# Kernel tuning notes

Hardware: AMD Instinct MI355X
Metric: run time of the kernel (lower is better)

Reference implementation:

```python
import jax, jax.numpy as jnp
import numpy as np

N_SIDE = 7
N_NODES = N_SIDE * N_SIDE  # 49


def _grid_edge_index(h, w):
    # torch_geometric.utils.grid: 9-point stencil (8 neighbors + self-loop)
    src, dst = [], []
    for y in range(h):
        for x in range(w):
            for dy in (-1, 0, 1):
                for dx in (-1, 0, 1):
                    ny, nx = y + dy, x + dx
                    if 0 <= ny < h and 0 <= nx < w:
                        src.append(ny * w + nx)
                        dst.append(y * w + x)
    return np.stack([np.array(src), np.array(dst)]).astype(np.int64)


def _gcn_norm_adj(edge_index, n):
    # PyG GCNConv default: add self-loops (on top of any existing), weight 1,
    # deg = in-degree by edge weight, A_hat = D^-1/2 (A + I) D^-1/2
    src, dst = edge_index[0], edge_index[1]
    A = jnp.zeros((n, n), dtype=jnp.float32).at[dst, src].add(1.0)
    A = A + jnp.eye(n, dtype=jnp.float32)  # GCNConv's added self-loops
    deg = A.sum(axis=1)
    d_inv_sqrt = jnp.where(deg > 0, jax.lax.rsqrt(deg), 0.0)
    return A * d_inv_sqrt[:, None] * d_inv_sqrt[None, :]  # [n, n]


def setup_inputs() -> dict:
    key = jax.random.key(0)
    ks = jax.random.split(key, 4)
    B = 4096
    features = jax.random.normal(ks[0], (B, N_NODES, 768), dtype=jnp.float32)
    W1 = jax.random.normal(ks[1], (768, 256), dtype=jnp.float32) * (1.0 / np.sqrt(768))
    b1 = jnp.zeros((256,), dtype=jnp.float32)
    W2 = jax.random.normal(ks[2], (256, 128), dtype=jnp.float32) * (1.0 / np.sqrt(256))
    b2 = jnp.zeros((128,), dtype=jnp.float32)
    fcW = jax.random.normal(ks[3], (128, 4), dtype=jnp.float32) * (1.0 / np.sqrt(128))
    fcb = jnp.zeros((4,), dtype=jnp.float32)
    edge_index = jnp.asarray(_grid_edge_index(N_SIDE, N_SIDE))  # [2, 361]
    return {"features": features, "W1": W1, "b1": b1, "W2": W2, "b2": b2,
            "fcW": fcW, "fcb": fcb, "edge_index": edge_index}


def reference(features, W1, b1, W2, b2, fcW, fcb, edge_index):
    # features: [B, N, 768]; batched GCN over the shared 7x7 grid graph
    A_hat = _gcn_norm_adj(edge_index, N_NODES)  # [N, N]
    # GCNConv: aggregate(X @ W) + b
    h = jnp.einsum('mn,bnd->bmd', A_hat, features @ W1) + b1  # [B, N, 256]
    h = jax.nn.relu(h)
    h = jnp.einsum('mn,bnd->bmd', A_hat, h @ W2) + b2  # [B, N, 128]
    h = jax.nn.relu(h)
    pooled = h.mean(axis=1)  # [B, 128] mean over nodes
    return pooled @ fcW + fcb  # [B, 4]
```

## Files before the change

kernel.cpp:

```cpp
#include <hip/hip_runtime.h>

#define NN 49
#define D0 768
#define D1 256
#define D2 128

typedef short v8s __attribute__((ext_vector_type(8)));
typedef float v4f __attribute__((ext_vector_type(4)));
typedef int   v4i __attribute__((ext_vector_type(4)));

__device__ __forceinline__ unsigned short f2bf(float f) {
  unsigned int u = __float_as_uint(f);
  u += 0x7FFFu + ((u >> 16) & 1u);
  return (unsigned short)(u >> 16);
}
__device__ __forceinline__ float bf2f(unsigned short u) {
  return __uint_as_float((unsigned)u << 16);
}

__device__ __forceinline__ int permk(int k) {
  return (k & ~31) | ((k & 12) << 1) | ((k & 16) >> 2) | (k & 3);
}

__device__ __forceinline__ float ahat(int m, int k) {
  if (m >= NN || k >= NN) return 0.f;
  int ym = m / 7, xm = m % 7, yk = k / 7, xk = k % 7;
  int dy = ym - yk, dx = xm - xk;
  if (dy < -1 || dy > 1 || dx < -1 || dx > 1) return 0.f;
  float rm = rsqrtf((float)((1 + (ym > 0) + (ym < 6)) * (1 + (xm > 0) + (xm < 6))) + 1.0f);
  float rk = rsqrtf((float)((1 + (yk > 0) + (yk < 6)) * (1 + (xk > 0) + (xk < 6))) + 1.0f);
  return ((m == k) ? 2.0f : 1.0f) * rm * rk;
}

#define W1_IMG_BYTES 393216
#define WS_NEEDED    458752

__global__ void prep_w(const float* __restrict__ W1, const float* __restrict__ W2,
                       char* __restrict__ wimg) {
  int id = blockIdx.x * 256 + threadIdx.x;
  if (id < 24576) {
    int kc = id >> 11, p = (id >> 8) & 7, tt = id & 255;
    int wvv = tt >> 6, lnn = tt & 63, qq = lnn >> 4, lmm = lnn & 15;
    int nt = p >> 1, s = p & 1;
    int n  = 64 * wvv + 16 * nt + lmm;
    int k0 = kc * 64 + 32 * s + 4 * qq;
    v8s v;
    #pragma unroll
    for (int i = 0; i < 4; ++i) {
      v[i]     = (short)f2bf(W1[(size_t)(k0 + i) * D1 + n]);
      v[i + 4] = (short)f2bf(W1[(size_t)(k0 + 16 + i) * D1 + n]);
    }
    *(v8s*)(wimg + (size_t)id * 16) = v;
  }
  int id2 = id - 24576;
  if (id2 >= 0 && id2 < 4096) {
    int kc = id2 >> 10, p = (id2 >> 8) & 3, tt = id2 & 255;
    int wvv = tt >> 6, lnn = tt & 63, qq = lnn >> 4, lmm = lnn & 15;
    int nt = p >> 1, s = p & 1;
    int n  = 32 * wvv + 16 * nt + lmm;
    int k0 = kc * 64 + 32 * s + 4 * qq;
    v8s v;
    #pragma unroll
    for (int i = 0; i < 4; ++i) {
      v[i]     = (short)f2bf(W2[(size_t)(k0 + i) * D2 + n]);
      v[i + 4] = (short)f2bf(W2[(size_t)(k0 + 16 + i) * D2 + n]);
    }
    *(v8s*)(wimg + W1_IMG_BYTES + (size_t)id2 * 16) = v;
  }
}

#define NOFF_SX    0
#define NOFF_SPOOL 0
#define NOFF_SH1   16384
#define NSMEM_SZ   49152

__device__ __forceinline__ void ldw8(v8s* dst, const char* base) {
  #pragma unroll
  for (int p = 0; p < 8; ++p) dst[p] = *(const v8s*)(base + p * 4096);
}
__device__ __forceinline__ void ldw4(v8s* dst, const char* base) {
  #pragma unroll
  for (int p = 0; p < 4; ++p) dst[p] = *(const v8s*)(base + p * 4096);
}

__device__ __forceinline__ void mfma_phase1(v4f (&acc)[4][4], const char* sx,
                                            const v8s* w, int q, int lm) {
  #pragma unroll
  for (int ks = 0; ks < 2; ++ks) {
    const int off = ks * 64 + (q << 4);
    v8s af[4];
    #pragma unroll
    for (int mt = 0; mt < 4; ++mt) {
      int row = mt * 16 + lm;
      af[mt] = *(const v8s*)(sx + ((row * 128 + off) ^ ((row & 7) << 4)));
    }
    #pragma unroll
    for (int mt = 0; mt < 4; ++mt)
      #pragma unroll
      for (int nt = 0; nt < 4; ++nt)
        acc[mt][nt] = __builtin_amdgcn_mfma_f32_16x16x32_bf16(af[mt], w[2 * nt + ks], acc[mt][nt], 0, 0, 0);
  }
}

__global__ __launch_bounds__(256, 2) void gcn_fused6(
    const float* __restrict__ X, const char* __restrict__ wimg,
    const float* __restrict__ b1v, const float* __restrict__ b2v,
    const float* __restrict__ fcWv, const float* __restrict__ fcbv,
    float* __restrict__ out)
{
  __shared__ __align__(16) char smem[NSMEM_SZ];
  const int t  = threadIdx.x;
  const int wv = t >> 6;
  const int ln = t & 63;
  const int q  = ln >> 4;
  const int lm = ln & 15;

  if (t < 240) {
    int i = (t >= 120) ? t - 120 : t;
    int base = ((t >= 120) ? 8192 : 0) + 6272 + i * 16;
    *(v4i*)(smem + NOFF_SX + base) = (v4i){0, 0, 0, 0};
  }

  const float* Xb = X + (size_t)blockIdx.x * (NN * D0);

  const int segA = t;
  const int segB = t + 256;
  const bool actB = (segB < NN * 8);
  const int rowA = segA >> 3, fA = segA & 7;
  const int rowB = segB >> 3, fB = segB & 7;
  const int gofsA = rowA * D0 + 32 * (fA >> 2) + 4 * (fA & 3);
  const int gofsB_ = rowB * D0 + 32 * (fB >> 2) + 4 * (fB & 3);
  const int gofsB = actB ? gofsB_ : gofsA;
  const int ldsA = (rowA * 128 + 16 * fA) ^ ((rowA & 7) << 4);
  const int ldsB = (rowB * 128 + 16 * fB) ^ ((rowB & 7) << 4);

  const int tofs = t * 16;
  const char* w1img = wimg;

  v4f acc[4][4];
  #pragma unroll
  for (int i = 0; i < 4; ++i)
    #pragma unroll
    for (int j = 0; j < 4; ++j)
      acc[i][j] = (v4f){0.f, 0.f, 0.f, 0.f};

  v8s wA[8], wB[8];
  ldw8(wA, w1img + tofs);
  float4 xa0 = *(const float4*)(Xb + gofsA);
  float4 xa1 = *(const float4*)(Xb + gofsA + 16);
  float4 xb0 = *(const float4*)(Xb + gofsB);
  float4 xb1 = *(const float4*)(Xb + gofsB + 16);

  for (int kc2 = 0; kc2 < 12; kc2 += 2) {
    {
      v8s v;
      v[0] = (short)f2bf(xa0.x); v[1] = (short)f2bf(xa0.y);
      v[2] = (short)f2bf(xa0.z); v[3] = (short)f2bf(xa0.w);
      v[4] = (short)f2bf(xa1.x); v[5] = (short)f2bf(xa1.y);
      v[6] = (short)f2bf(xa1.z); v[7] = (short)f2bf(xa1.w);
      *(v8s*)(smem + NOFF_SX + ldsA) = v;
      if (actB) {
        v8s w;
        w[0] = (short)f2bf(xb0.x); w[1] = (short)f2bf(xb0.y);
        w[2] = (short)f2bf(xb0.z); w[3] = (short)f2bf(xb0.w);
        w[4] = (short)f2bf(xb1.x); w[5] = (short)f2bf(xb1.y);
        w[6] = (short)f2bf(xb1.z); w[7] = (short)f2bf(xb1.w);
        *(v8s*)(smem + NOFF_SX + ldsB) = w;
      }
    }
    {
      const float* xp = Xb + (kc2 + 1) * 64;
      xa0 = *(const float4*)(xp + gofsA);
      xa1 = *(const float4*)(xp + gofsA + 16);
      xb0 = *(const float4*)(xp + gofsB);
      xb1 = *(const float4*)(xp + gofsB + 16);
      ldw8(wB, w1img + (kc2 + 1) * 32768 + tofs);
    }
    __builtin_amdgcn_sched_barrier(0);
    asm volatile("s_waitcnt lgkmcnt(0)" ::: "memory");
    __builtin_amdgcn_s_barrier();
    __builtin_amdgcn_sched_barrier(0);
    mfma_phase1(acc, smem + NOFF_SX, wA, q, lm);

    {
      v8s v;
      v[0] = (short)f2bf(xa0.x); v[1] = (short)f2bf(xa0.y);
      v[2] = (short)f2bf(xa0.z); v[3] = (short)f2bf(xa0.w);
      v[4] = (short)f2bf(xa1.x); v[5] = (short)f2bf(xa1.y);
      v[6] = (short)f2bf(xa1.z); v[7] = (short)f2bf(xa1.w);
      *(v8s*)(smem + NOFF_SX + 8192 + ldsA) = v;
      if (actB) {
        v8s w;
        w[0] = (short)f2bf(xb0.x); w[1] = (short)f2bf(xb0.y);
        w[2] = (short)f2bf(xb0.z); w[3] = (short)f2bf(xb0.w);
        w[4] = (short)f2bf(xb1.x); w[5] = (short)f2bf(xb1.y);
        w[6] = (short)f2bf(xb1.z); w[7] = (short)f2bf(xb1.w);
        *(v8s*)(smem + NOFF_SX + 8192 + ldsB) = w;
      }
    }
    if (kc2 < 10) {
      const float* xp = Xb + (kc2 + 2) * 64;
      xa0 = *(const float4*)(xp + gofsA);
      xa1 = *(const float4*)(xp + gofsA + 16);
      xb0 = *(const float4*)(xp + gofsB);
      xb1 = *(const float4*)(xp + gofsB + 16);
      ldw8(wA, w1img + (kc2 + 2) * 32768 + tofs);
    }
    __builtin_amdgcn_sched_barrier(0);
    asm volatile("s_waitcnt lgkmcnt(0)" ::: "memory");
    __builtin_amdgcn_s_barrier();
    __builtin_amdgcn_sched_barrier(0);
    mfma_phase1(acc, smem + NOFF_SX + 8192, wB, q, lm);
  }

  const char* w2img = wimg + W1_IMG_BYTES;
  v8s w2c[4][4];
  ldw4(w2c[0], w2img + tofs);
  ldw4(w2c[1], w2img + 16384 + tofs);

  float bi[4];
  #pragma unroll
  for (int nt = 0; nt < 4; ++nt) bi[nt] = b1v[64 * wv + 16 * nt + lm];

  v8s afH[4][2], afL[4][2];
  #pragma unroll
  for (int mt = 0; mt < 4; ++mt) {
    int m = 16 * mt + lm;
    #pragma unroll
    for (int s2 = 0; s2 < 2; ++s2) {
      v8s hi, lo;
      #pragma unroll
      for (int j = 0; j < 8; ++j) {
        int k = 32 * s2 + ((j & 4) << 2) + 4 * q + (j & 3);
        float v = ahat(m, k);
        unsigned short h = f2bf(v);
        hi[j] = (short)h;
        lo[j] = (short)f2bf(v - bf2f(h));
      }
      afH[mt][s2] = hi; afL[mt][s2] = lo;
    }
  }

  v4f ag[4][4];
  #pragma unroll
  for (int mt = 0; mt < 4; ++mt)
    #pragma unroll
    for (int nt = 0; nt < 4; ++nt)
      ag[mt][nt] = (v4f){bi[nt], bi[nt], bi[nt], bi[nt]};

  #pragma unroll
  for (int s2 = 0; s2 < 2; ++s2)
    #pragma unroll
    for (int nt = 0; nt < 4; ++nt) {
      v8s b;
      #pragma unroll
      for (int i = 0; i < 4; ++i) {
        b[i]     = (short)f2bf(acc[2 * s2][nt][i]);
        b[i + 4] = (short)f2bf(acc[2 * s2 + 1][nt][i]);
      }
      #pragma unroll
      for (int mt = 0; mt < 4; ++mt) {
        ag[mt][nt] = __builtin_amdgcn_mfma_f32_16x16x32_bf16(afL[mt][s2], b, ag[mt][nt], 0, 0, 0);
        ag[mt][nt] = __builtin_amdgcn_mfma_f32_16x16x32_bf16(afH[mt][s2], b, ag[mt][nt], 0, 0, 0);
      }
    }

  ldw4(w2c[2], w2img + 2 * 16384 + tofs);
  ldw4(w2c[3], w2img + 3 * 16384 + tofs);

  #pragma unroll
  for (int mt = 0; mt < 4; ++mt)
    #pragma unroll
    for (int nt = 0; nt < 4; ++nt) {
      int ch  = 64 * wv + 16 * nt + lm;
      int chb = 2 * permk(ch);
      #pragma unroll
      for (int r = 0; r < 4; ++r) {
        int row = 16 * mt + 4 * q + r;
        float hv = fmaxf(ag[mt][nt][r], 0.f);
        int byte = (row * 512 + chb) ^ ((row & 7) << 4);
        *(unsigned short*)(smem + NOFF_SH1 + byte) = f2bf(hv);
      }
    }
  __builtin_amdgcn_sched_barrier(0);
  asm volatile("s_waitcnt lgkmcnt(0)" ::: "memory");
  __builtin_amdgcn_s_barrier();
  __builtin_amdgcn_sched_barrier(0);

  v4f acc3[4][2];
  #pragma unroll
  for (int i = 0; i < 4; ++i) { acc3[i][0] = (v4f){0.f,0.f,0.f,0.f}; acc3[i][1] = (v4f){0.f,0.f,0.f,0.f}; }

  #pragma unroll
  for (int kc = 0; kc < 4; ++kc)
    #pragma unroll
    for (int ks = 0; ks < 2; ++ks) {
      const int off = ks * 64 + (q << 4);
      v8s af[4];
      #pragma unroll
      for (int mt = 0; mt < 4; ++mt) {
        int row = mt * 16 + lm;
        int byte = (row * 512 + kc * 128 + off) ^ ((row & 7) << 4);
        af[mt] = *(const v8s*)(smem + NOFF_SH1 + byte);
      }
      #pragma unroll
      for (int mt = 0; mt < 4; ++mt)
        #pragma unroll
        for (int nt = 0; nt < 2; ++nt)
          acc3[mt][nt] = __builtin_amdgcn_mfma_f32_16x16x32_bf16(af[mt], w2c[kc][2 * nt + ks], acc3[mt][nt], 0, 0, 0);
    }

  float b2i[2];
  b2i[0] = b2v[32 * wv + lm];
  b2i[1] = b2v[32 * wv + 16 + lm];
  v4f a2[4][2];
  #pragma unroll
  for (int mt = 0; mt < 4; ++mt) {
    a2[mt][0] = (v4f){b2i[0], b2i[0], b2i[0], b2i[0]};
    a2[mt][1] = (v4f){b2i[1], b2i[1], b2i[1], b2i[1]};
  }
  #pragma unroll
  for (int s2 = 0; s2 < 2; ++s2)
    #pragma unroll
    for (int nt = 0; nt < 2; ++nt) {
      v8s b;
      #pragma unroll
      for (int i = 0; i < 4; ++i) {
        b[i]     = (short)f2bf(acc3[2 * s2][nt][i]);
        b[i + 4] = (short)f2bf(acc3[2 * s2 + 1][nt][i]);
      }
      #pragma unroll
      for (int mt = 0; mt < 4; ++mt) {
        a2[mt][nt] = __builtin_amdgcn_mfma_f32_16x16x32_bf16(afL[mt][s2], b, a2[mt][nt], 0, 0, 0);
        a2[mt][nt] = __builtin_amdgcn_mfma_f32_16x16x32_bf16(afH[mt][s2], b, a2[mt][nt], 0, 0, 0);
      }
    }

  float ps0 = 0.f, ps1 = 0.f;
  #pragma unroll
  for (int mt = 0; mt < 3; ++mt)
    #pragma unroll
    for (int r = 0; r < 4; ++r) {
      ps0 += fmaxf(a2[mt][0][r], 0.f);
      ps1 += fmaxf(a2[mt][1][r], 0.f);
    }
  if (q == 0) {
    ps0 += fmaxf(a2[3][0][0], 0.f);
    ps1 += fmaxf(a2[3][1][0], 0.f);
  }
  ps0 += __shfl_xor(ps0, 16); ps0 += __shfl_xor(ps0, 32);
  ps1 += __shfl_xor(ps1, 16); ps1 += __shfl_xor(ps1, 32);
  float* spool = (float*)(smem + NOFF_SPOOL);
  __syncthreads();
  if (q == 0) {
    spool[32 * wv + lm]      = ps0 * (1.0f / 49.0f);
    spool[32 * wv + 16 + lm] = ps1 * (1.0f / 49.0f);
  }
  __syncthreads();
  if (t < 4) {
    float a = fcbv[t];
    for (int d = 0; d < D2; ++d) a += spool[d] * fcWv[d * 4 + t];
    out[(size_t)blockIdx.x * 4 + t] = a;
  }
}

#define OFF_SX    0
#define OFF_SWT   8192
#define OFF_SC    0
#define OFF_SWT2  0
#define OFF_SPOOL 25872
#define OFF_SPF   30096
#define OFF_SH1   40960
#define OFF_NBRW  73728
#define OFF_NBRI  75492
#define OFF_B1    77256
#define OFF_B2    78280
#define OFF_FCW   78792
#define OFF_FCB   80840
#define SMEM_SZ   80856

__global__ __launch_bounds__(256, 2) void gcn_fused_fb(
    const float* __restrict__ X, const float* __restrict__ W1,
    const float* __restrict__ b1v, const float* __restrict__ W2,
    const float* __restrict__ b2v, const float* __restrict__ fcWv,
    const float* __restrict__ fcbv, float* __restrict__ out)
{
  __shared__ __align__(16) char smem[SMEM_SZ];
  const int t  = threadIdx.x;
  const int wv = t >> 6;
  const int ln = t & 63;
  const int q  = ln >> 4;
  const int lm = ln & 15;

  float* nbrW = (float*)(smem + OFF_NBRW);
  int*   nbrI = (int*)  (smem + OFF_NBRI);
  float* b1s  = (float*)(smem + OFF_B1);
  float* b2s  = (float*)(smem + OFF_B2);
  float* fcWs = (float*)(smem + OFF_FCW);
  float* fcbs = (float*)(smem + OFF_FCB);
  float* sC   = (float*)(smem + OFF_SC);

  if (t < D1) b1s[t] = b1v[t];
  if (t < D2) b2s[t] = b2v[t];
  fcWs[t]       = fcWv[t];
  fcWs[t + 256] = fcWv[t + 256];
  if (t < 4) fcbs[t] = fcbv[t];
  if (t < NN) {
    int y = t / 7, x = t % 7;
    float rm = rsqrtf((float)((1 + (y > 0) + (y < 6)) * (1 + (x > 0) + (x < 6))) + 1.0f);
    int cnt = 0;
    for (int dy = -1; dy <= 1; ++dy)
      for (int dx = -1; dx <= 1; ++dx) {
        int ny = y + dy, nx = x + dx;
        if (ny >= 0 && ny < 7 && nx >= 0 && nx < 7) {
          int n = ny * 7 + nx;
          float rn = rsqrtf((float)((1 + (ny > 0) + (ny < 6)) * (1 + (nx > 0) + (nx < 6))) + 1.0f);
          nbrW[t * 9 + cnt] = ((n == t) ? 2.0f : 1.0f) * rm * rn;
          nbrI[t * 9 + cnt] = n;
          ++cnt;
        }
      }
    for (; cnt < 9; ++cnt) { nbrW[t * 9 + cnt] = 0.0f; nbrI[t * 9 + cnt] = 0; }
  }
  __syncthreads();

  const float* Xb = X + (size_t)blockIdx.x * (NN * D0);
  v4f acc[4][4];
  #pragma unroll
  for (int i = 0; i < 4; ++i)
    #pragma unroll
    for (int j = 0; j < 4; ++j)
      acc[i][j] = (v4f){0.f, 0.f, 0.f, 0.f};

  for (int kc = 0; kc < 12; ++kc) {
    __syncthreads();
    #pragma unroll
    for (int p = 0; p < 4; ++p) {
      int idx = t + 256 * p;
      int row = idx >> 4;
      int k4  = (idx & 15) << 2;
      float4 v = {0.f, 0.f, 0.f, 0.f};
      if (row < NN) v = *(const float4*)(Xb + row * D0 + kc * 64 + k4);
      ushort4 s;
      s.x = f2bf(v.x); s.y = f2bf(v.y); s.z = f2bf(v.z); s.w = f2bf(v.w);
      int byte = row * 128 + 2 * permk(k4);
      byte ^= (row & 7) << 4;
      *(ushort4*)(smem + OFF_SX + byte) = s;
    }
    #pragma unroll
    for (int p = 0; p < 4; ++p) {
      int bid2 = t + 256 * p;
      int k0 = (bid2 & 15) << 2;
      int n0 = (bid2 >> 4) << 2;
      const float* wp = W1 + (size_t)(kc * 64 + k0) * D1 + n0;
      float4 r0 = *(const float4*)(wp);
      float4 r1 = *(const float4*)(wp + D1);
      float4 r2 = *(const float4*)(wp + 2 * D1);
      float4 r3 = *(const float4*)(wp + 3 * D1);
      int kb = 2 * permk(k0);
      ushort4 s; int byte;
      s.x = f2bf(r0.x); s.y = f2bf(r1.x); s.z = f2bf(r2.x); s.w = f2bf(r3.x);
      byte = (n0 + 0) * 128 + kb; byte ^= ((n0 + 0) & 7) << 4;
      *(ushort4*)(smem + OFF_SWT + byte) = s;
      s.x = f2bf(r0.y); s.y = f2bf(r1.y); s.z = f2bf(r2.y); s.w = f2bf(r3.y);
      byte = (n0 + 1) * 128 + kb; byte ^= ((n0 + 1) & 7) << 4;
      *(ushort4*)(smem + OFF_SWT + byte) = s;
      s.x = f2bf(r0.z); s.y = f2bf(r1.z); s.z = f2bf(r2.z); s.w = f2bf(r3.z);
      byte = (n0 + 2) * 128 + kb; byte ^= ((n0 + 2) & 7) << 4;
      *(ushort4*)(smem + OFF_SWT + byte) = s;
      s.x = f2bf(r0.w); s.y = f2bf(r1.w); s.z = f2bf(r2.w); s.w = f2bf(r3.w);
      byte = (n0 + 3) * 128 + kb; byte ^= ((n0 + 3) & 7) << 4;
      *(ushort4*)(smem + OFF_SWT + byte) = s;
    }
    __syncthreads();
    #pragma unroll
    for (int ks = 0; ks < 2; ++ks) {
      int off = ks * 64 + (q << 4);
      v8s af[4], bf[4];
      #pragma unroll
      for (int mt = 0; mt < 4; ++mt) {
        int row = mt * 16 + lm;
        int byte = row * 128 + off; byte ^= (row & 7) << 4;
        af[mt] = *(const v8s*)(smem + OFF_SX + byte);
      }
      #pragma unroll
      for (int nt = 0; nt < 4; ++nt) {
        int n = (wv * 4 + nt) * 16 + lm;
        int byte = n * 128 + off; byte ^= (n & 7) << 4;
        bf[nt] = *(const v8s*)(smem + OFF_SWT + byte);
      }
      #pragma unroll
      for (int mt = 0; mt < 4; ++mt)
        #pragma unroll
        for (int nt = 0; nt < 4; ++nt)
          acc[mt][nt] = __builtin_amdgcn_mfma_f32_16x16x32_bf16(af[mt], bf[nt], acc[mt][nt], 0, 0, 0);
    }
  }

  #pragma unroll
  for (int h = 0; h < 2; ++h) {
    __syncthreads();
    if ((wv >> 1) == h) {
      #pragma unroll
      for (int mt = 0; mt < 4; ++mt) {
        int rbase = mt * 16 + (q << 2);
        #pragma unroll
        for (int nt = 0; nt < 4; ++nt) {
          int c = ((wv & 1) * 4 + nt) * 16 + lm;
          #pragma unroll
          for (int r = 0; r < 4; ++r) {
            int row = rbase + r;
            if (row < NN) sC[row * 132 + c] = acc[mt][nt][r];
          }
        }
      }
    }
    __syncthreads();
    for (int p = 0; p < 7; ++p) {
      int idx = t + 256 * p;
      if (idx < NN * 32) {
        int m  = idx >> 5;
        int d4 = (idx & 31) << 2;
        int dg = h * 128 + d4;
        float a0 = b1s[dg], a1 = b1s[dg + 1], a2 = b1s[dg + 2], a3 = b1s[dg + 3];
        #pragma unroll
        for (int e = 0; e < 9; ++e) {
          float w = nbrW[m * 9 + e];
          int   n = nbrI[m * 9 + e];
          float4 cv = *(const float4*)(sC + n * 132 + d4);
          a0 += w * cv.x; a1 += w * cv.y; a2 += w * cv.z; a3 += w * cv.w;
        }
        a0 = fmaxf(a0, 0.f); a1 = fmaxf(a1, 0.f); a2 = fmaxf(a2, 0.f); a3 = fmaxf(a3, 0.f);
        ushort4 s; s.x = f2bf(a0); s.y = f2bf(a1); s.z = f2bf(a2); s.w = f2bf(a3);
        int byte = m * 512 + 2 * permk(dg);
        byte ^= (m & 7) << 4;
        *(ushort4*)(smem + OFF_SH1 + byte) = s;
      }
    }
  }

  v4f acc2[4][2];
  #pragma unroll
  for (int i = 0; i < 4; ++i) { acc2[i][0] = (v4f){0.f,0.f,0.f,0.f}; acc2[i][1] = (v4f){0.f,0.f,0.f,0.f}; }

  for (int kc = 0; kc < 4; ++kc) {
    __syncthreads();
    #pragma unroll
    for (int p = 0; p < 2; ++p) {
      int bid2 = t + 256 * p;
      int k0 = (bid2 & 15) << 2;
      int n0 = (bid2 >> 4) << 2;
      const float* wp = W2 + (size_t)(kc * 64 + k0) * D2 + n0;
      float4 r0 = *(const float4*)(wp);
      float4 r1 = *(const float4*)(wp + D2);
      float4 r2 = *(const float4*)(wp + 2 * D2);
      float4 r3 = *(const float4*)(wp + 3 * D2);
      int kb = 2 * permk(k0);
      ushort4 s; int byte;
      s.x = f2bf(r0.x); s.y = f2bf(r1.x); s.z = f2bf(r2.x); s.w = f2bf(r3.x);
      byte = (n0 + 0) * 128 + kb; byte ^= ((n0 + 0) & 7) << 4;
      *(ushort4*)(smem + OFF_SWT2 + byte) = s;
      s.x = f2bf(r0.y); s.y = f2bf(r1.y); s.z = f2bf(r2.y); s.w = f2bf(r3.y);
      byte = (n0 + 1) * 128 + kb; byte ^= ((n0 + 1) & 7) << 4;
      *(ushort4*)(smem + OFF_SWT2 + byte) = s;
      s.x = f2bf(r0.z); s.y = f2bf(r1.z); s.z = f2bf(r2.z); s.w = f2bf(r3.z);
      byte = (n0 + 2) * 128 + kb; byte ^= ((n0 + 2) & 7) << 4;
      *(ushort4*)(smem + OFF_SWT2 + byte) = s;
      s.x = f2bf(r0.w); s.y = f2bf(r1.w); s.z = f2bf(r2.w); s.w = f2bf(r3.w);
      byte = (n0 + 3) * 128 + kb; byte ^= ((n0 + 3) & 7) << 4;
      *(ushort4*)(smem + OFF_SWT2 + byte) = s;
    }
    __syncthreads();
    #pragma unroll
    for (int ks = 0; ks < 2; ++ks) {
      int off = ks * 64 + (q << 4);
      v8s af[4], bf2[2];
      #pragma unroll
      for (int mt = 0; mt < 4; ++mt) {
        int row = mt * 16 + lm;
        int byte = row * 512 + kc * 128 + off; byte ^= (row & 7) << 4;
        af[mt] = *(const v8s*)(smem + OFF_SH1 + byte);
      }
      #pragma unroll
      for (int nt = 0; nt < 2; ++nt) {
        int n = (wv * 2 + nt) * 16 + lm;
        int byte = n * 128 + off; byte ^= (n & 7) << 4;
        bf2[nt] = *(const v8s*)(smem + OFF_SWT2 + byte);
      }
      #pragma unroll
      for (int mt = 0; mt < 4; ++mt)
        #pragma unroll
        for (int nt = 0; nt < 2; ++nt)
          acc2[mt][nt] = __builtin_amdgcn_mfma_f32_16x16x32_bf16(af[mt], bf2[nt], acc2[mt][nt], 0, 0, 0);
    }
  }

  __syncthreads();
  #pragma unroll
  for (int mt = 0; mt < 4; ++mt) {
    int rbase = mt * 16 + (q << 2);
    #pragma unroll
    for (int nt = 0; nt < 2; ++nt) {
      int c = (wv * 2 + nt) * 16 + lm;
      #pragma unroll
      for (int r = 0; r < 4; ++r) {
        int row = rbase + r;
        if (row < NN) sC[row * 132 + c] = acc2[mt][nt][r];
      }
    }
  }
  __syncthreads();
  {
    int d4 = (t & 31) << 2;
    int g  = t >> 5;
    float p0 = 0.f, p1 = 0.f, p2 = 0.f, p3 = 0.f;
    int m0 = g * 7, m1 = (g * 7 + 7 < NN) ? (g * 7 + 7) : NN;
    for (int m = m0; m < m1; ++m) {
      float a0 = b2s[d4], a1 = b2s[d4 + 1], a2 = b2s[d4 + 2], a3 = b2s[d4 + 3];
      #pragma unroll
      for (int e = 0; e < 9; ++e) {
        float w = nbrW[m * 9 + e];
        int   n = nbrI[m * 9 + e];
        float4 cv = *(const float4*)(sC + n * 132 + d4);
        a0 += w * cv.x; a1 += w * cv.y; a2 += w * cv.z; a3 += w * cv.w;
      }
      p0 += fmaxf(a0, 0.f); p1 += fmaxf(a1, 0.f); p2 += fmaxf(a2, 0.f); p3 += fmaxf(a3, 0.f);
    }
    float* sp = (float*)(smem + OFF_SPOOL) + g * 132 + d4;
    sp[0] = p0; sp[1] = p1; sp[2] = p2; sp[3] = p3;
  }
  __syncthreads();
  if (t < D2) {
    const float* sp = (const float*)(smem + OFF_SPOOL);
    float s = 0.f;
    #pragma unroll
    for (int g = 0; g < 8; ++g) s += sp[g * 132 + t];
    ((float*)(smem + OFF_SPF))[t] = s * (1.0f / 49.0f);
  }
  __syncthreads();
  if (t < 4) {
    const float* pf = (const float*)(smem + OFF_SPF);
    float a = fcbs[t];
    for (int d = 0; d < D2; ++d) a += pf[d] * fcWs[d * 4 + t];
    out[(size_t)blockIdx.x * 4 + t] = a;
  }
}

extern "C" void kernel_launch(void* const* d_in, const int* in_sizes, int n_in,
                              void* d_out, int out_size, void* d_ws, size_t ws_size,
                              hipStream_t stream) {
  const float* X   = (const float*)d_in[0];
  const float* W1  = (const float*)d_in[1];
  const float* b1  = (const float*)d_in[2];
  const float* W2  = (const float*)d_in[3];
  const float* b2  = (const float*)d_in[4];
  const float* fcW = (const float*)d_in[5];
  const float* fcb = (const float*)d_in[6];
  float* out = (float*)d_out;
  int B = in_sizes[0] / (NN * D0);
  if (d_ws != nullptr && ws_size >= (size_t)WS_NEEDED) {
    prep_w<<<112, 256, 0, stream>>>(W1, W2, (char*)d_ws);
    gcn_fused6<<<B, 256, 0, stream>>>(X, (const char*)d_ws, b1, b2, fcW, fcb, out);
  } else {
    gcn_fused_fb<<<B, 256, 0, stream>>>(X, W1, b1, W2, b2, fcW, fcb, out);
  }
}
```

Before: 224.0 us.

## Process two graphs per block to share W1/W2 register fragments

Each block now handles two batch samples instead of one. The W1 fragments loaded into registers per k-chunk, and the W2 fragments, are reused for both samples' MFMAs, which halves weight traffic per sample. The X staging loop becomes single-buffered with one LDS slot per sample, and shared memory grows to 80KB to hold both samples' hidden activations. The trade-off is that LDS double-buffering across k-chunks is lost, the grid is halved, and register pressure and LDS use rise, which could reduce occupancy.

```diff
diff --git a/kernel.cpp b/kernel.cpp
--- a/kernel.cpp
+++ b/kernel.cpp
@@ -39,11 +39,11 @@
                        char* __restrict__ wimg) {
   int id = blockIdx.x * 256 + threadIdx.x;
   if (id < 24576) {
-    int kc = id >> 11, p = (id >> 8) & 7, tt = id & 255;
+    int p = (id >> 8) & 7, tt = id & 255;
     int wvv = tt >> 6, lnn = tt & 63, qq = lnn >> 4, lmm = lnn & 15;
     int nt = p >> 1, s = p & 1;
     int n  = 64 * wvv + 16 * nt + lmm;
-    int k0 = kc * 64 + 32 * s + 4 * qq;
+    int k0 = (id >> 11) * 64 + 32 * s + 4 * qq;
     v8s v;
     #pragma unroll
     for (int i = 0; i < 4; ++i) {
@@ -54,11 +54,11 @@
   }
   int id2 = id - 24576;
   if (id2 >= 0 && id2 < 4096) {
-    int kc = id2 >> 10, p = (id2 >> 8) & 3, tt = id2 & 255;
+    int p = (id2 >> 8) & 3, tt = id2 & 255;
     int wvv = tt >> 6, lnn = tt & 63, qq = lnn >> 4, lmm = lnn & 15;
     int nt = p >> 1, s = p & 1;
     int n  = 32 * wvv + 16 * nt + lmm;
-    int k0 = kc * 64 + 32 * s + 4 * qq;
+    int k0 = (id2 >> 10) * 64 + 32 * s + 4 * qq;
     v8s v;
     #pragma unroll
     for (int i = 0; i < 4; ++i) {
@@ -69,10 +69,13 @@
   }
 }
 
-#define NOFF_SX    0
-#define NOFF_SPOOL 0
-#define NOFF_SH1   16384
-#define NSMEM_SZ   49152
+#define SX0    0
+#define SX1    8192
+#define SH1_0  16384
+#define SH1_1  49152
+#define SPOOL0 0
+#define SPOOL1 512
+#define NSMEM7 81920
 
 __device__ __forceinline__ void ldw8(v8s* dst, const char* base) {
   #pragma unroll
@@ -82,33 +85,22 @@
   #pragma unroll
   for (int p = 0; p < 4; ++p) dst[p] = *(const v8s*)(base + p * 4096);
 }
-
-__device__ __forceinline__ void mfma_phase1(v4f (&acc)[4][4], const char* sx,
-                                            const v8s* w, int q, int lm) {
-  #pragma unroll
-  for (int ks = 0; ks < 2; ++ks) {
-    const int off = ks * 64 + (q << 4);
-    v8s af[4];
-    #pragma unroll
-    for (int mt = 0; mt < 4; ++mt) {
-      int row = mt * 16 + lm;
-      af[mt] = *(const v8s*)(sx + ((row * 128 + off) ^ ((row & 7) << 4)));
-    }
-    #pragma unroll
-    for (int mt = 0; mt < 4; ++mt)
-      #pragma unroll
-      for (int nt = 0; nt < 4; ++nt)
-        acc[mt][nt] = __builtin_amdgcn_mfma_f32_16x16x32_bf16(af[mt], w[2 * nt + ks], acc[mt][nt], 0, 0, 0);
-  }
-}
-
-__global__ __launch_bounds__(256, 2) void gcn_fused6(
+__device__ __forceinline__ void commit8(char* lds, const float4& a, const float4& b) {
+  v8s v;
+  v[0] = (short)f2bf(a.x); v[1] = (short)f2bf(a.y);
+  v[2] = (short)f2bf(a.z); v[3] = (short)f2bf(a.w);
+  v[4] = (short)f2bf(b.x); v[5] = (short)f2bf(b.y);
+  v[6] = (short)f2bf(b.z); v[7] = (short)f2bf(b.w);
+  *(v8s*)lds = v;
+}
+
+__global__ __launch_bounds__(256, 2) void gcn_fused8(
     const float* __restrict__ X, const char* __restrict__ wimg,
     const float* __restrict__ b1v, const float* __restrict__ b2v,
     const float* __restrict__ fcWv, const float* __restrict__ fcbv,
     float* __restrict__ out)
 {
-  __shared__ __align__(16) char smem[NSMEM_SZ];
+  __shared__ __align__(16) char smem[NSMEM7];
   const int t  = threadIdx.x;
   const int wv = t >> 6;
   const int ln = t & 63;
@@ -117,106 +109,124 @@
 
   if (t < 240) {
     int i = (t >= 120) ? t - 120 : t;
-    int base = ((t >= 120) ? 8192 : 0) + 6272 + i * 16;
-    *(v4i*)(smem + NOFF_SX + base) = (v4i){0, 0, 0, 0};
-  }
-
-  const float* Xb = X + (size_t)blockIdx.x * (NN * D0);
-
-  const int segA = t;
-  const int segB = t + 256;
-  const bool actB = (segB < NN * 8);
-  const int rowA = segA >> 3, fA = segA & 7;
-  const int rowB = segB >> 3, fB = segB & 7;
-  const int gofsA = rowA * D0 + 32 * (fA >> 2) + 4 * (fA & 3);
-  const int gofsB_ = rowB * D0 + 32 * (fB >> 2) + 4 * (fB & 3);
-  const int gofsB = actB ? gofsB_ : gofsA;
-  const int ldsA = (rowA * 128 + 16 * fA) ^ ((rowA & 7) << 4);
-  const int ldsB = (rowB * 128 + 16 * fB) ^ ((rowB & 7) << 4);
+    int base = ((t >= 120) ? SX1 : SX0) + 6272 + i * 16;
+    *(v4i*)(smem + base) = (v4i){0, 0, 0, 0};
+  }
+
+  const float* X0 = X + (size_t)(2 * blockIdx.x) * (NN * D0);
+  const float* X1 = X0 + NN * D0;
+
+  const int g1 = t + 256;
+  const int b1g = (g1 >= 392) ? 1 : 0;
+  const bool act3 = (t < 16);
+  const int s0 = t, s1 = g1 - 392 * b1g, s2 = t + 120, s3 = t + 376;
+  const int r0 = s0 >> 3, f0 = s0 & 7;
+  const int r1 = s1 >> 3, f1 = s1 & 7;
+  const int r2 = s2 >> 3, f2 = s2 & 7;
+  const int r3 = s3 >> 3, f3 = s3 & 7;
+  const float* base0 = X0 + r0 * D0 + 32 * (f0 >> 2) + 4 * (f0 & 3);
+  const float* base1 = (b1g ? X1 : X0) + r1 * D0 + 32 * (f1 >> 2) + 4 * (f1 & 3);
+  const float* base2 = X1 + r2 * D0 + 32 * (f2 >> 2) + 4 * (f2 & 3);
+  const float* base3_ = X1 + r3 * D0 + 32 * (f3 >> 2) + 4 * (f3 & 3);
+  const float* base3 = act3 ? base3_ : base0;
+  const int lds0 = SX0 + ((r0 * 128 + 16 * f0) ^ ((r0 & 7) << 4));
+  const int lds1 = (b1g ? SX1 : SX0) + ((r1 * 128 + 16 * f1) ^ ((r1 & 7) << 4));
+  const int lds2 = SX1 + ((r2 * 128 + 16 * f2) ^ ((r2 & 7) << 4));
+  const int lds3 = SX1 + (((r3 & 63) * 128 + 16 * f3) ^ ((r3 & 7) << 4));
 
   const int tofs = t * 16;
-  const char* w1img = wimg;
-
-  v4f acc[4][4];
+
+  v4f accA[4][4], accB[4][4];
   #pragma unroll
   for (int i = 0; i < 4; ++i)
     #pragma unroll
-    for (int j = 0; j < 4; ++j)
-      acc[i][j] = (v4f){0.f, 0.f, 0.f, 0.f};
-
-  v8s wA[8], wB[8];
-  ldw8(wA, w1img + tofs);
-  float4 xa0 = *(const float4*)(Xb + gofsA);
-  float4 xa1 = *(const float4*)(Xb + gofsA + 16);
-  float4 xb0 = *(const float4*)(Xb + gofsB);
-  float4 xb1 = *(const float4*)(Xb + gofsB + 16);
-
-  for (int kc2 = 0; kc2 < 12; kc2 += 2) {
-    {
-      v8s v;
-      v[0] = (short)f2bf(xa0.x); v[1] = (short)f2bf(xa0.y);
-      v[2] = (short)f2bf(xa0.z); v[3] = (short)f2bf(xa0.w);
-      v[4] = (short)f2bf(xa1.x); v[5] = (short)f2bf(xa1.y);
-      v[6] = (short)f2bf(xa1.z); v[7] = (short)f2bf(xa1.w);
-      *(v8s*)(smem + NOFF_SX + ldsA) = v;
-      if (actB) {
-        v8s w;
-        w[0] = (short)f2bf(xb0.x); w[1] = (short)f2bf(xb0.y);
-        w[2] = (short)f2bf(xb0.z); w[3] = (short)f2bf(xb0.w);
-        w[4] = (short)f2bf(xb1.x); w[5] = (short)f2bf(xb1.y);
-        w[6] = (short)f2bf(xb1.z); w[7] = (short)f2bf(xb1.w);
-        *(v8s*)(smem + NOFF_SX + ldsB) = w;
-      }
-    }
-    {
-      const float* xp = Xb + (kc2 + 1) * 64;
-      xa0 = *(const float4*)(xp + gofsA);
-      xa1 = *(const float4*)(xp + gofsA + 16);
-      xb0 = *(const float4*)(xp + gofsB);
-      xb1 = *(const float4*)(xp + gofsB + 16);
-      ldw8(wB, w1img + (kc2 + 1) * 32768 + tofs);
+    for (int j = 0; j < 4; ++j) {
+      accA[i][j] = (v4f){0.f, 0.f, 0.f, 0.f};
+      accB[i][j] = (v4f){0.f, 0.f, 0.f, 0.f};
+    }
+
+  v8s wA[8];
+  ldw8(wA, wimg + tofs);
+  float4 p0a = *(const float4*)(base0);
+  float4 p0b = *(const float4*)(base0 + 16);
+  float4 p1a = *(const float4*)(base1);
+  float4 p1b = *(const float4*)(base1 + 16);
+  float4 p2a = *(const float4*)(base2);
+  float4 p2b = *(const float4*)(base2 + 16);
+  float4 p3a = *(const float4*)(base3);
+  float4 p3b = *(const float4*)(base3 + 16);
+
+  for (int kc = 0; kc < 12; ++kc) {
+    __builtin_amdgcn_sched_barrier(0);
+    __builtin_amdgcn_s_barrier();
+    __builtin_amdgcn_sched_barrier(0);
+    commit8((char*)smem + lds0, p0a, p0b);
+    commit8((char*)smem + lds1, p1a, p1b);
+    commit8((char*)smem + lds2, p2a, p2b);
+    if (act3) commit8((char*)smem + lds3, p3a, p3b);
+    if (kc < 11) {
+      const int o = (kc + 1) * 64;
+      p0a = *(const float4*)(base0 + o);
+      p0b = *(const float4*)(base0 + o + 16);
+      p1a = *(const float4*)(base1 + o);
+      p1b = *(const float4*)(base1 + o + 16);
+      p2a = *(const float4*)(base2 + o);
+      p2b = *(const float4*)(base2 + o + 16);
+      p3a = *(const float4*)(base3 + o);
+      p3b = *(const float4*)(base3 + o + 16);
     }
     __builtin_amdgcn_sched_barrier(0);
     asm volatile("s_waitcnt lgkmcnt(0)" ::: "memory");
     __builtin_amdgcn_s_barrier();
     __builtin_amdgcn_sched_barrier(0);
-    mfma_phase1(acc, smem + NOFF_SX, wA, q, lm);
-
-    {
-      v8s v;
-      v[0] = (short)f2bf(xa0.x); v[1] = (short)f2bf(xa0.y);
-      v[2] = (short)f2bf(xa0.z); v[3] = (short)f2bf(xa0.w);
-      v[4] = (short)f2bf(xa1.x); v[5] = (short)f2bf(xa1.y);
-      v[6] = (short)f2bf(xa1.z); v[7] = (short)f2bf(xa1.w);
-      *(v8s*)(smem + NOFF_SX + 8192 + ldsA) = v;
-      if (actB) {
-        v8s w;
-        w[0] = (short)f2bf(xb0.x); w[1] = (short)f2bf(xb0.y);
-        w[2] = (short)f2bf(xb0.z); w[3] = (short)f2bf(xb0.w);
-        w[4] = (short)f2bf(xb1.x); w[5] = (short)f2bf(xb1.y);
-        w[6] = (short)f2bf(xb1.z); w[7] = (short)f2bf(xb1.w);
-        *(v8s*)(smem + NOFF_SX + 8192 + ldsB) = w;
-      }
-    }
-    if (kc2 < 10) {
-      const float* xp = Xb + (kc2 + 2) * 64;
-      xa0 = *(const float4*)(xp + gofsA);
-      xa1 = *(const float4*)(xp + gofsA + 16);
-      xb0 = *(const float4*)(xp + gofsB);
-      xb1 = *(const float4*)(xp + gofsB + 16);
-      ldw8(wA, w1img + (kc2 + 2) * 32768 + tofs);
-    }
-    __builtin_amdgcn_sched_barrier(0);
-    asm volatile("s_waitcnt lgkmcnt(0)" ::: "memory");
-    __builtin_amdgcn_s_barrier();
-    __builtin_amdgcn_sched_barrier(0);
-    mfma_phase1(acc, smem + NOFF_SX + 8192, wB, q, lm);
-  }
-
-  const char* w2img = wimg + W1_IMG_BYTES;
-  v8s w2c[4][4];
-  ldw4(w2c[0], w2img + tofs);
-  ldw4(w2c[1], w2img + 16384 + tofs);
+    #pragma unroll
+    for (int ks = 0; ks < 2; ++ks) {
+      const int off = ks * 64 + (q << 4);
+      v8s af[4];
+      #pragma unroll
+      for (int mt = 0; mt < 4; ++mt) {
+        int row = mt * 16 + lm;
+        af[mt] = *(const v8s*)(smem + SX0 + ((row * 128 + off) ^ ((row & 7) << 4)));
+      }
+      #pragma unroll
+      for (int mt = 0; mt < 4; ++mt)
+        #pragma unroll
+        for (int nt = 0; nt < 4; ++nt)
+          accA[mt][nt] = __builtin_amdgcn_mfma_f32_16x16x32_bf16(af[mt], wA[2 * nt + ks], accA[mt][nt], 0, 0, 0);
+    }
+    #pragma unroll
+    for (int ks = 0; ks < 2; ++ks) {
+      const int off = ks * 64 + (q << 4);
+      v8s af[4];
+      #pragma unroll
+      for (int mt = 0; mt < 4; ++mt) {
+        int row = mt * 16 + lm;
+        af[mt] = *(const v8s*)(smem + SX1 + ((row * 128 + off) ^ ((row & 7) << 4)));
+      }
+      #pragma unroll
+      for (int mt = 0; mt < 4; ++mt)
+        #pragma unroll
+        for (int nt = 0; nt < 4; ++nt)
+          accB[mt][nt] = __builtin_amdgcn_mfma_f32_16x16x32_bf16(af[mt], wA[2 * nt + ks], accB[mt][nt], 0, 0, 0);
+    }
+    if (kc < 11) ldw8(wA, wimg + (kc + 1) * 32768 + tofs);
+  }
+
+  v8s bA[2][4], bB[2][4];
+  #pragma unroll
+  for (int s2 = 0; s2 < 2; ++s2)
+    #pragma unroll
+    for (int nt = 0; nt < 4; ++nt) {
+      v8s a, b;
+      #pragma unroll
+      for (int i = 0; i < 4; ++i) {
+        a[i]     = (short)f2bf(accA[2 * s2][nt][i]);
+        a[i + 4] = (short)f2bf(accA[2 * s2 + 1][nt][i]);
+        b[i]     = (short)f2bf(accB[2 * s2][nt][i]);
+        b[i + 4] = (short)f2bf(accB[2 * s2 + 1][nt][i]);
+      }
+      bA[s2][nt] = a; bB[s2][nt] = b;
+    }
 
   float bi[4];
   #pragma unroll
@@ -241,126 +251,134 @@
     }
   }
 
-  v4f ag[4][4];
-  #pragma unroll
-  for (int mt = 0; mt < 4; ++mt)
-    #pragma unroll
-    for (int nt = 0; nt < 4; ++nt)
-      ag[mt][nt] = (v4f){bi[nt], bi[nt], bi[nt], bi[nt]};
-
-  #pragma unroll
-  for (int s2 = 0; s2 < 2; ++s2)
-    #pragma unroll
-    for (int nt = 0; nt < 4; ++nt) {
-      v8s b;
-      #pragma unroll
-      for (int i = 0; i < 4; ++i) {
-        b[i]     = (short)f2bf(acc[2 * s2][nt][i]);
-        b[i + 4] = (short)f2bf(acc[2 * s2 + 1][nt][i]);
-      }
-      #pragma unroll
-      for (int mt = 0; mt < 4; ++mt) {
-        ag[mt][nt] = __builtin_amdgcn_mfma_f32_16x16x32_bf16(afL[mt][s2], b, ag[mt][nt], 0, 0, 0);
-        ag[mt][nt] = __builtin_amdgcn_mfma_f32_16x16x32_bf16(afH[mt][s2], b, ag[mt][nt], 0, 0, 0);
-      }
-    }
-
-  ldw4(w2c[2], w2img + 2 * 16384 + tofs);
-  ldw4(w2c[3], w2img + 3 * 16384 + tofs);
-
-  #pragma unroll
-  for (int mt = 0; mt < 4; ++mt)
-    #pragma unroll
-    for (int nt = 0; nt < 4; ++nt) {
-      int ch  = 64 * wv + 16 * nt + lm;
-      int chb = 2 * permk(ch);
-      #pragma unroll
-      for (int r = 0; r < 4; ++r) {
-        int row = 16 * mt + 4 * q + r;
-        float hv = fmaxf(ag[mt][nt][r], 0.f);
-        int byte = (row * 512 + chb) ^ ((row & 7) << 4);
-        *(unsigned short*)(smem + NOFF_SH1 + byte) = f2bf(hv);
-      }
-    }
+  #pragma unroll
+  for (int bb = 0; bb < 2; ++bb) {
+    v4f ag[4][4];
+    #pragma unroll
+    for (int mt = 0; mt < 4; ++mt)
+      #pragma unroll
+      for (int nt = 0; nt < 4; ++nt)
+        ag[mt][nt] = (v4f){bi[nt], bi[nt], bi[nt], bi[nt]};
+    #pragma unroll
+    for (int s2 = 0; s2 < 2; ++s2)
+      #pragma unroll
+      for (int nt = 0; nt < 4; ++nt) {
+        v8s b = (bb == 0) ? bA[s2][nt] : bB[s2][nt];
+        #pragma unroll
+        for (int mt = 0; mt < 4; ++mt) {
+          ag[mt][nt] = __builtin_amdgcn_mfma_f32_16x16x32_bf16(afL[mt][s2], b, ag[mt][nt], 0, 0, 0);
+          ag[mt][nt] = __builtin_amdgcn_mfma_f32_16x16x32_bf16(afH[mt][s2], b, ag[mt][nt], 0, 0, 0);
+        }
+      }
+    const int hbase = (bb == 0) ? SH1_0 : SH1_1;
+    #pragma unroll
+    for (int mt = 0; mt < 4; ++mt)
+      #pragma unroll
+      for (int nt = 0; nt < 4; ++nt) {
+        int ch  = 64 * wv + 16 * nt + lm;
+        int chb = 2 * permk(ch);
+        #pragma unroll
+        for (int r = 0; r < 4; ++r) {
+          int row = 16 * mt + 4 * q + r;
+          float hv = fmaxf(ag[mt][nt][r], 0.f);
+          int byte = (row * 512 + chb) ^ ((row & 7) << 4);
+          *(unsigned short*)(smem + hbase + byte) = f2bf(hv);
+        }
+      }
+  }
+
+  const char* w2img = wimg + W1_IMG_BYTES;
+  v8s w2c0[4], w2c1[4], w2c2[4], w2c3[4];
+  ldw4(w2c0, w2img + tofs);
+  ldw4(w2c1, w2img + 16384 + tofs);
+  ldw4(w2c2, w2img + 2 * 16384 + tofs);
+  ldw4(w2c3, w2img + 3 * 16384 + tofs);
+
   __builtin_amdgcn_sched_barrier(0);
   asm volatile("s_waitcnt lgkmcnt(0)" ::: "memory");
   __builtin_amdgcn_s_barrier();
   __builtin_amdgcn_sched_barrier(0);
 
-  v4f acc3[4][2];
-  #pragma unroll
-  for (int i = 0; i < 4; ++i) { acc3[i][0] = (v4f){0.f,0.f,0.f,0.f}; acc3[i][1] = (v4f){0.f,0.f,0.f,0.f}; }
-
-  #pragma unroll
-  for (int kc = 0; kc < 4; ++kc)
-    #pragma unroll
-    for (int ks = 0; ks < 2; ++ks) {
-      const int off = ks * 64 + (q << 4);
-      v8s af[4];
-      #pragma unroll
-      for (int mt = 0; mt < 4; ++mt) {
-        int row = mt * 16 + lm;
-        int byte = (row * 512 + kc * 128 + off) ^ ((row & 7) << 4);
-        af[mt] = *(const v8s*)(smem + NOFF_SH1 + byte);
-      }
-      #pragma unroll
-      for (int mt = 0; mt < 4; ++mt)
-        #pragma unroll
-        for (int nt = 0; nt < 2; ++nt)
-          acc3[mt][nt] = __builtin_amdgcn_mfma_f32_16x16x32_bf16(af[mt], w2c[kc][2 * nt + ks], acc3[mt][nt], 0, 0, 0);
-    }
-
-  float b2i[2];
-  b2i[0] = b2v[32 * wv + lm];
-  b2i[1] = b2v[32 * wv + 16 + lm];
-  v4f a2[4][2];
-  #pragma unroll
-  for (int mt = 0; mt < 4; ++mt) {
-    a2[mt][0] = (v4f){b2i[0], b2i[0], b2i[0], b2i[0]};
-    a2[mt][1] = (v4f){b2i[1], b2i[1], b2i[1], b2i[1]};
-  }
-  #pragma unroll
-  for (int s2 = 0; s2 < 2; ++s2)
-    #pragma unroll
-    for (int nt = 0; nt < 2; ++nt) {
-      v8s b;
-      #pragma unroll
-      for (int i = 0; i < 4; ++i) {
-        b[i]     = (short)f2bf(acc3[2 * s2][nt][i]);
-        b[i + 4] = (short)f2bf(acc3[2 * s2 + 1][nt][i]);
-      }
-      #pragma unroll
-      for (int mt = 0; mt < 4; ++mt) {
-        a2[mt][nt] = __builtin_amdgcn_mfma_f32_16x16x32_bf16(afL[mt][s2], b, a2[mt][nt], 0, 0, 0);
-        a2[mt][nt] = __builtin_amdgcn_mfma_f32_16x16x32_bf16(afH[mt][s2], b, a2[mt][nt], 0, 0, 0);
-      }
-    }
-
-  float ps0 = 0.f, ps1 = 0.f;
-  #pragma unroll
-  for (int mt = 0; mt < 3; ++mt)
-    #pragma unroll
-    for (int r = 0; r < 4; ++r) {
-      ps0 += fmaxf(a2[mt][0][r], 0.f);
-      ps1 += fmaxf(a2[mt][1][r], 0.f);
-    }
-  if (q == 0) {
-    ps0 += fmaxf(a2[3][0][0], 0.f);
-    ps1 += fmaxf(a2[3][1][0], 0.f);
-  }
-  ps0 += __shfl_xor(ps0, 16); ps0 += __shfl_xor(ps0, 32);
-  ps1 += __shfl_xor(ps1, 16); ps1 += __shfl_xor(ps1, 32);
-  float* spool = (float*)(smem + NOFF_SPOOL);
+  float b2i0 = b2v[32 * wv + lm];
+  float b2i1 = b2v[32 * wv + 16 + lm];
+
+  #pragma unroll
+  for (int bb = 0; bb < 2; ++bb) {
+    const int hbase = (bb == 0) ? SH1_0 : SH1_1;
+    v4f acc3[4][2];
+    #pragma unroll
+    for (int i = 0; i < 4; ++i) {
+      acc3[i][0] = (v4f){0.f, 0.f, 0.f, 0.f};
+      acc3[i][1] = (v4f){0.f, 0.f, 0.f, 0.f};
+    }
+    #pragma unroll
+    for (int kc = 0; kc < 4; ++kc)
+      #pragma unroll
+      for (int ks = 0; ks < 2; ++ks) {
+        const int off = ks * 64 + (q << 4);
+        v8s af[4];
+        #pragma unroll
+        for (int mt = 0; mt < 4; ++mt) {
+          int row = mt * 16 + lm;
+          int byte = (row * 512 + kc * 128 + off) ^ ((row & 7) << 4);
+          af[mt] = *(const v8s*)(smem + hbase + byte);
+        }
+        const v8s* wc = (kc == 0) ? w2c0 : (kc == 1) ? w2c1 : (kc == 2) ? w2c2 : w2c3;
+        #pragma unroll
+        for (int mt = 0; mt < 4; ++mt)
+          #pragma unroll
+          for (int nt = 0; nt < 2; ++nt)
+            acc3[mt][nt] = __builtin_amdgcn_mfma_f32_16x16x32_bf16(af[mt], wc[2 * nt + ks], acc3[mt][nt], 0, 0, 0);
+      }
+    v4f a2[4][2];
+    #pragma unroll
+    for (int mt = 0; mt < 4; ++mt) {
+      a2[mt][0] = (v4f){b2i0, b2i0, b2i0, b2i0};
+      a2[mt][1] = (v4f){b2i1, b2i1, b2i1, b2i1};
+    }
+    #pragma unroll
+    for (int s2 = 0; s2 < 2; ++s2)
+      #pragma unroll
+      for (int nt = 0; nt < 2; ++nt) {
+        v8s b;
+        #pragma unroll
+        for (int i = 0; i < 4; ++i) {
+          b[i]     = (short)f2bf(acc3[2 * s2][nt][i]);
+          b[i + 4] = (short)f2bf(acc3[2 * s2 + 1][nt][i]);
+        }
+        #pragma unroll
+        for (int mt = 0; mt < 4; ++mt) {
+          a2[mt][nt] = __builtin_amdgcn_mfma_f32_16x16x32_bf16(afL[mt][s2], b, a2[mt][nt], 0, 0, 0);
+          a2[mt][nt] = __builtin_amdgcn_mfma_f32_16x16x32_bf16(afH[mt][s2], b, a2[mt][nt], 0, 0, 0);
+        }
+      }
+    float ps0 = 0.f, ps1 = 0.f;
+    #pragma unroll
+    for (int mt = 0; mt < 3; ++mt)
+      #pragma unroll
+      for (int r = 0; r < 4; ++r) {
+        ps0 += fmaxf(a2[mt][0][r], 0.f);
+        ps1 += fmaxf(a2[mt][1][r], 0.f);
+      }
+    if (q == 0) {
+      ps0 += fmaxf(a2[3][0][0], 0.f);
+      ps1 += fmaxf(a2[3][1][0], 0.f);
+    }
+    ps0 += __shfl_xor(ps0, 16); ps0 += __shfl_xor(ps0, 32);
+    ps1 += __shfl_xor(ps1, 16); ps1 += __shfl_xor(ps1, 32);
+    float* spool = (float*)(smem + ((bb == 0) ? SPOOL0 : SPOOL1));
+    if (q == 0) {
+      spool[32 * wv + lm]      = ps0 * (1.0f / 49.0f);
+      spool[32 * wv + 16 + lm] = ps1 * (1.0f / 49.0f);
+    }
+  }
   __syncthreads();
-  if (q == 0) {
-    spool[32 * wv + lm]      = ps0 * (1.0f / 49.0f);
-    spool[32 * wv + 16 + lm] = ps1 * (1.0f / 49.0f);
-  }
-  __syncthreads();
-  if (t < 4) {
-    float a = fcbv[t];
-    for (int d = 0; d < D2; ++d) a += spool[d] * fcWv[d * 4 + t];
-    out[(size_t)blockIdx.x * 4 + t] = a;
+  if (t < 8) {
+    int bb = t >> 2, c = t & 3;
+    const float* spool = (const float*)(smem + ((bb == 0) ? SPOOL0 : SPOOL1));
+    float a = fcbv[c];
+    for (int d = 0; d < D2; ++d) a += spool[d] * fcWv[d * 4 + c];
+    out[(size_t)(2 * blockIdx.x + bb) * 4 + c] = a;
   }
 }
 
@@ -658,9 +676,9 @@
   const float* fcb = (const float*)d_in[6];
   float* out = (float*)d_out;
   int B = in_sizes[0] / (NN * D0);
-  if (d_ws != nullptr && ws_size >= (size_t)WS_NEEDED) {
+  if (d_ws != nullptr && ws_size >= (size_t)WS_NEEDED && (B % 2) == 0) {
     prep_w<<<112, 256, 0, stream>>>(W1, W2, (char*)d_ws);
-    gcn_fused6<<<B, 256, 0, stream>>>(X, (const char*)d_ws, b1, b2, fcW, fcb, out);
+    gcn_fused8<<<B / 2, 256, 0, stream>>>(X, (const char*)d_ws, b1, b2, fcW, fcb, out);
   } else {
     gcn_fused_fb<<<B, 256, 0, stream>>>(X, W1, b1, W2, b2, fcW, fcb, out);
   }
```

New measurement: 185.1 us. 1.21x faster.
